# Performance work log

Hardware: AMD Instinct MI355X
Metric: run time of the kernel (lower is better)

Reference implementation:

```python
import jax, jax.numpy as jnp
import numpy as np

N_NODES = 50000
N_EDGES = 600000
H_DIM = 128
BN_EPS = 1e-5


def setup_inputs() -> dict:
    key = jax.random.key(0)
    k1, k2, k3, k4 = jax.random.split(key, 4)
    ent_emb = jax.random.normal(k1, (N_NODES, H_DIM), dtype=jnp.float32)
    # xavier_normal_ init for the 128x128 weight
    std = float(np.sqrt(2.0 / (H_DIM + H_DIM)))
    neigh_w = jax.random.normal(k2, (H_DIM, H_DIM), dtype=jnp.float32) * std
    gamma = jnp.ones((H_DIM,), dtype=jnp.float32)
    beta = jnp.zeros((H_DIM,), dtype=jnp.float32)
    src = jax.random.randint(k3, (N_EDGES,), 0, N_NODES, dtype=jnp.int32)
    dst = jax.random.randint(k4, (N_EDGES,), 0, N_NODES, dtype=jnp.int32)
    return {"ent_emb": ent_emb, "neigh_w": neigh_w, "gamma": gamma,
            "beta": beta, "src": src, "dst": dst}


def reference(ent_emb, neigh_w, gamma, beta, src, dst):
    # Edge dot-product scores: u_dot_v('emb','emb')  -> [E]
    e_src = ent_emb[src]                      # [E, H]
    e_dst = ent_emb[dst]                      # [E, H]
    scores = jnp.sum(e_src * e_dst, axis=-1)  # [E]

    # edge_softmax: softmax over incoming edges of each destination node
    seg_max = jax.ops.segment_max(scores, dst, num_segments=N_NODES)
    seg_max = jnp.where(jnp.isfinite(seg_max), seg_max, 0.0)  # nodes w/o edges
    e = jnp.exp(scores - seg_max[dst])                         # [E]
    seg_sum = jax.ops.segment_sum(e, dst, num_segments=N_NODES)
    norm = e / seg_sum[dst]                                    # [E]

    # update_all(u_mul_e, sum): weighted gather-sum aggregation
    msg = e_src * norm[:, None]                                # [E, H]
    neigh = jax.ops.segment_sum(msg, dst, num_segments=N_NODES)  # [N, H]

    # matmul + BatchNorm1d (training-mode batch stats) + tanh
    h = neigh @ neigh_w                                        # [N, H]
    mean = jnp.mean(h, axis=0)
    var = jnp.var(h, axis=0)  # biased, matches torch BN normalization
    h = (h - mean) * jax.lax.rsqrt(var + BN_EPS) * gamma + beta
    return jnp.tanh(h)
```

## Files before the change

### kernel.cpp

```cpp
#include <hip/hip_runtime.h>
#include <hip/hip_fp16.h>
#include <math.h>

#define N_NODES 50000
#define N_EDGES 600000
#define H 128
#define BN_EPS 1e-5f
#define MAXDEG 48

__global__ void k_scatter(const int* __restrict__ src, const int* __restrict__ dst,
                          int* __restrict__ cnt, int* __restrict__ slots) {
    int i = blockIdx.x * blockDim.x + threadIdx.x;
    if (i < N_EDGES) {
        int d = dst[i];
        int pos = atomicAdd(cnt + d, 1);
        if (pos < MAXDEG) slots[d * MAXDEG + pos] = src[i];
    }
}

#define F4SCALE(a, s) { (a).x *= (s); (a).y *= (s); (a).z *= (s); (a).w *= (s); }
#define F4FMA(a, e, v) { (a).x += (e)*(v).x; (a).y += (e)*(v).y; (a).z += (e)*(v).z; (a).w += (e)*(v).w; }
#define F4SHFLADD(a, msk) { (a).x += __shfl_xor((a).x, msk, 64); (a).y += __shfl_xor((a).y, msk, 64); \
                            (a).z += __shfl_xor((a).z, msk, 64); (a).w += __shfl_xor((a).w, msk, 64); }

__global__ __launch_bounds__(256) void k_fused(const float* __restrict__ emb,
                                               const int* __restrict__ cnt,
                                               const int* __restrict__ slots,
                                               float* __restrict__ neigh) {
    int wid = (blockIdx.x * blockDim.x + threadIdx.x) >> 6;
    int lane = threadIdx.x & 63;
    if (wid >= N_NODES) return;
    int g = lane >> 3;
    int l = lane & 7;

    int deg = min(cnt[wid], MAXDEG);
    int sid = slots[wid * MAXDEG + min(lane, MAXDEG - 1)];

    const float4* rd = (const float4*)(emb + (size_t)wid * H) + l * 4;
    float4 b0 = rd[0], b1 = rd[1], b2 = rd[2], b3 = rd[3];

    float m = -INFINITY, ssum = 0.0f;
    float4 acc0 = {0,0,0,0}, acc1 = {0,0,0,0}, acc2 = {0,0,0,0}, acc3 = {0,0,0,0};

    for (int cb = 0; cb < deg; cb += 8) {
        int e = cb + g;
        bool valid = e < deg;
        int s = __shfl(sid, valid ? e : 0, 64);
        const float4* rs = (const float4*)(emb + (size_t)s * H) + l * 4;
        float4 a0 = rs[0], a1 = rs[1], a2 = rs[2], a3 = rs[3];

        float v = a0.x*b0.x + a0.y*b0.y + a0.z*b0.z + a0.w*b0.w
                + a1.x*b1.x + a1.y*b1.y + a1.z*b1.z + a1.w*b1.w
                + a2.x*b2.x + a2.y*b2.y + a2.z*b2.z + a2.w*b2.w
                + a3.x*b3.x + a3.y*b3.y + a3.z*b3.z + a3.w*b3.w;
        v += __shfl_xor(v, 1, 64);
        v += __shfl_xor(v, 2, 64);
        v += __shfl_xor(v, 4, 64);
        if (!valid) v = -INFINITY;

        float cmax = v;
        cmax = fmaxf(cmax, __shfl_xor(cmax, 8, 64));
        cmax = fmaxf(cmax, __shfl_xor(cmax, 16, 64));
        cmax = fmaxf(cmax, __shfl_xor(cmax, 32, 64));
        float mnew = fmaxf(m, cmax);
        if (mnew > m) {
            float scale = __expf(m - mnew);
            ssum *= scale;
            F4SCALE(acc0, scale); F4SCALE(acc1, scale);
            F4SCALE(acc2, scale); F4SCALE(acc3, scale);
            m = mnew;
        }

        float ev = __expf(v - m);
        ssum += ev;
        F4FMA(acc0, ev, a0); F4FMA(acc1, ev, a1);
        F4FMA(acc2, ev, a2); F4FMA(acc3, ev, a3);
    }

    ssum += __shfl_xor(ssum, 8, 64);
    ssum += __shfl_xor(ssum, 16, 64);
    ssum += __shfl_xor(ssum, 32, 64);
    F4SHFLADD(acc0, 8);  F4SHFLADD(acc1, 8);  F4SHFLADD(acc2, 8);  F4SHFLADD(acc3, 8);
    F4SHFLADD(acc0, 16); F4SHFLADD(acc1, 16); F4SHFLADD(acc2, 16); F4SHFLADD(acc3, 16);
    F4SHFLADD(acc0, 32); F4SHFLADD(acc1, 32); F4SHFLADD(acc2, 32); F4SHFLADD(acc3, 32);

    float inv = (deg > 0) ? 1.0f / ssum : 0.0f;
    if (g == 0) {
        float4* po = (float4*)(neigh + (size_t)wid * H) + l * 4;
        F4SCALE(acc0, inv); F4SCALE(acc1, inv); F4SCALE(acc2, inv); F4SCALE(acc3, inv);
        po[0] = acc0; po[1] = acc1; po[2] = acc2; po[3] = acc3;
    }
}

#define MM_ROWS 128
#define MM_COLS 64
template <bool F16>
__global__ __launch_bounds__(256, 4) void k_matmul(const float* __restrict__ neigh,
                                                   const float* __restrict__ W,
                                                   float* __restrict__ hout32,
                                                   __half* __restrict__ hout16,
                                                   float* __restrict__ stats) {
    __shared__ float Wl[H * MM_COLS];
    __shared__ float Sl[16 * MM_COLS];
    __shared__ float Ql[16 * MM_COLS];
    int t = threadIdx.x;
    int bc = blockIdx.x & 1;
    int br = blockIdx.x >> 1;
    int c0 = bc * MM_COLS;
    int n0 = br * MM_ROWS;
    int cg = t & 15, rg = t >> 4;
    int j0 = cg * 4;
    int r0 = n0 + rg * 8;

    for (int idx = t; idx < H * 16; idx += 256) {
        int k = idx >> 4, c4 = idx & 15;
        *(float4*)&Wl[k * MM_COLS + c4 * 4] =
            *((const float4*)(W + (size_t)k * H + c0) + c4);
    }

    const float* pr[8];
    bool valid[8];
#pragma unroll
    for (int i = 0; i < 8; ++i) {
        int n = r0 + i;
        valid[i] = (n < N_NODES);
        pr[i] = neigh + (size_t)(valid[i] ? n : 0) * H;
    }

    __syncthreads();

    float acc[8][4] = {};
    for (int k0 = 0; k0 < H; k0 += 4) {
        float4 rv[8];
#pragma unroll
        for (int i = 0; i < 8; ++i) rv[i] = *(const float4*)(pr[i] + k0);
        float4 wv[4];
#pragma unroll
        for (int kk = 0; kk < 4; ++kk) wv[kk] = *(const float4*)&Wl[(k0 + kk) * MM_COLS + j0];
#pragma unroll
        for (int kk = 0; kk < 4; ++kk) {
#pragma unroll
            for (int i = 0; i < 8; ++i) {
                float rk = ((const float*)&rv[i])[kk];
                acc[i][0] += rk * wv[kk].x;
                acc[i][1] += rk * wv[kk].y;
                acc[i][2] += rk * wv[kk].z;
                acc[i][3] += rk * wv[kk].w;
            }
        }
    }

#pragma unroll
    for (int i = 0; i < 8; ++i) {
        if (valid[i]) {
            if (F16) {
                __half2 h01 = __floats2half2_rn(acc[i][0], acc[i][1]);
                __half2 h23 = __floats2half2_rn(acc[i][2], acc[i][3]);
                __half2* p = (__half2*)(hout16 + (size_t)(r0 + i) * H + c0 + j0);
                p[0] = h01; p[1] = h23;
            } else {
                float4 o = make_float4(acc[i][0], acc[i][1], acc[i][2], acc[i][3]);
                *(float4*)(hout32 + (size_t)(r0 + i) * H + c0 + j0) = o;
            }
        }
    }

#pragma unroll
    for (int c = 0; c < 4; ++c) {
        float s = 0.0f, q = 0.0f;
#pragma unroll
        for (int i = 0; i < 8; ++i) {
            if (valid[i]) { s += acc[i][c]; q += acc[i][c] * acc[i][c]; }
        }
        Sl[rg * MM_COLS + j0 + c] = s;
        Ql[rg * MM_COLS + j0 + c] = q;
    }
    __syncthreads();
    if (t < MM_COLS) {
        float s = 0.0f;
#pragma unroll
        for (int r = 0; r < 16; ++r) s += Sl[r * MM_COLS + t];
        atomicAdd(stats + c0 + t, s);
    } else if (t < 2 * MM_COLS) {
        int j = t - MM_COLS;
        float q = 0.0f;
#pragma unroll
        for (int r = 0; r < 16; ++r) q += Ql[r * MM_COLS + j];
        atomicAdd(stats + 128 + c0 + j, q);
    }
}

__device__ __forceinline__ float tanh_fast(float x) {
    float e = __expf(2.0f * x);
    return 1.0f - 2.0f / (e + 1.0f);
}

__global__ __launch_bounds__(256) void k_apply_f32(float* __restrict__ h,
                                                   const float* __restrict__ stats,
                                                   const float* __restrict__ gamma,
                                                   const float* __restrict__ beta) {
    __shared__ float sc[128], sh[128];
    int t = threadIdx.x;
    if (t < 128) {
        float mean = stats[t] * (1.0f / N_NODES);
        float var = stats[128 + t] * (1.0f / N_NODES) - mean * mean;
        var = fmaxf(var, 0.0f);
        float s = gamma[t] * rsqrtf(var + BN_EPS);
        sc[t] = s;
        sh[t] = beta[t] - mean * s;
    }
    __syncthreads();
    int i = blockIdx.x * 256 + t;
    if (i < N_NODES * H / 4) {
        float4 v = ((const float4*)h)[i];
        int jb = (i & 31) * 4;
        v.x = tanh_fast(v.x * sc[jb]     + sh[jb]);
        v.y = tanh_fast(v.y * sc[jb + 1] + sh[jb + 1]);
        v.z = tanh_fast(v.z * sc[jb + 2] + sh[jb + 2]);
        v.w = tanh_fast(v.w * sc[jb + 3] + sh[jb + 3]);
        ((float4*)h)[i] = v;
    }
}

__global__ __launch_bounds__(256) void k_apply_f16(const __half* __restrict__ h,
                                                   float* __restrict__ out,
                                                   const float* __restrict__ stats,
                                                   const float* __restrict__ gamma,
                                                   const float* __restrict__ beta) {
    __shared__ float sc[128], sh[128];
    int t = threadIdx.x;
    if (t < 128) {
        float mean = stats[t] * (1.0f / N_NODES);
        float var = stats[128 + t] * (1.0f / N_NODES) - mean * mean;
        var = fmaxf(var, 0.0f);
        float s = gamma[t] * rsqrtf(var + BN_EPS);
        sc[t] = s;
        sh[t] = beta[t] - mean * s;
    }
    __syncthreads();
    int i = blockIdx.x * 256 + t;
    if (i < N_NODES * H / 8) {
        union { uint4 u; __half2 h2[4]; } U;
        U.u = ((const uint4*)h)[i];
        int jb = (i & 15) * 8;
        float2 f0 = __half22float2(U.h2[0]);
        float2 f1 = __half22float2(U.h2[1]);
        float2 f2 = __half22float2(U.h2[2]);
        float2 f3 = __half22float2(U.h2[3]);
        float4 o0, o1;
        o0.x = tanh_fast(f0.x * sc[jb]     + sh[jb]);
        o0.y = tanh_fast(f0.y * sc[jb + 1] + sh[jb + 1]);
        o0.z = tanh_fast(f1.x * sc[jb + 2] + sh[jb + 2]);
        o0.w = tanh_fast(f1.y * sc[jb + 3] + sh[jb + 3]);
        o1.x = tanh_fast(f2.x * sc[jb + 4] + sh[jb + 4]);
        o1.y = tanh_fast(f2.y * sc[jb + 5] + sh[jb + 5]);
        o1.z = tanh_fast(f3.x * sc[jb + 6] + sh[jb + 6]);
        o1.w = tanh_fast(f3.y * sc[jb + 7] + sh[jb + 7]);
        ((float4*)out)[2 * i]     = o0;
        ((float4*)out)[2 * i + 1] = o1;
    }
}

extern "C" void kernel_launch(void* const* d_in, const int* in_sizes, int n_in,
                              void* d_out, int out_size, void* d_ws, size_t ws_size,
                              hipStream_t stream) {
    const float* emb   = (const float*)d_in[0];
    const float* W     = (const float*)d_in[1];
    const float* gamma = (const float*)d_in[2];
    const float* beta  = (const float*)d_in[3];
    const int*   src   = (const int*)d_in[4];
    const int*   dst   = (const int*)d_in[5];
    float* out = (float*)d_out;

    int*    cnt   = (int*)d_ws;
    float*  stats = (float*)(cnt + N_NODES);
    int*    slots = (int*)(stats + 256) + 4;
    float*  neigh = (float*)(slots + (size_t)N_NODES * MAXDEG);
    __half* hbuf  = (__half*)(neigh + (size_t)N_NODES * H);

    size_t need_f16 = (size_t)(N_NODES + 260) * 4
                    + (size_t)N_NODES * MAXDEG * 4
                    + (size_t)N_NODES * H * 4
                    + (size_t)N_NODES * H * 2;
    bool use_f16 = ws_size >= need_f16;

    hipMemsetAsync(cnt, 0, (N_NODES + 260) * sizeof(int), stream);
    k_scatter<<<(N_EDGES + 255) / 256, 256, 0, stream>>>(src, dst, cnt, slots);
    k_fused<<<(N_NODES * 64 + 255) / 256, 256, 0, stream>>>(emb, cnt, slots, neigh);

    int nblk_mm = ((N_NODES + MM_ROWS - 1) / MM_ROWS) * 2;
    if (use_f16) {
        k_matmul<true><<<nblk_mm, 256, 0, stream>>>(neigh, W, nullptr, hbuf, stats);
        k_apply_f16<<<(N_NODES * H / 8 + 255) / 256, 256, 0, stream>>>(hbuf, out, stats, gamma, beta);
    } else {
        k_matmul<false><<<nblk_mm, 256, 0, stream>>>(neigh, W, out, nullptr, stats);
        k_apply_f32<<<(N_NODES * H / 4 + 255) / 256, 256, 0, stream>>>(out, stats, gamma, beta);
    }
}
```

Measured before the change: 217.5 us.

## Compute all 128 output columns per matmul block to halve neigh reads

```diff
diff --git a/kernel.cpp b/kernel.cpp
--- a/kernel.cpp
+++ b/kernel.cpp
@@ -93,30 +93,21 @@
 }
 
 #define MM_ROWS 128
-#define MM_COLS 64
 template <bool F16>
-__global__ __launch_bounds__(256, 4) void k_matmul(const float* __restrict__ neigh,
+__global__ __launch_bounds__(256, 2) void k_matmul(const float* __restrict__ neigh,
                                                    const float* __restrict__ W,
                                                    float* __restrict__ hout32,
                                                    __half* __restrict__ hout16,
                                                    float* __restrict__ stats) {
-    __shared__ float Wl[H * MM_COLS];
-    __shared__ float Sl[16 * MM_COLS];
-    __shared__ float Ql[16 * MM_COLS];
+    __shared__ float Wl[H * H];
     int t = threadIdx.x;
-    int bc = blockIdx.x & 1;
-    int br = blockIdx.x >> 1;
-    int c0 = bc * MM_COLS;
-    int n0 = br * MM_ROWS;
+    int n0 = blockIdx.x * MM_ROWS;
     int cg = t & 15, rg = t >> 4;
-    int j0 = cg * 4;
+    int j0 = cg * 8;
     int r0 = n0 + rg * 8;
 
-    for (int idx = t; idx < H * 16; idx += 256) {
-        int k = idx >> 4, c4 = idx & 15;
-        *(float4*)&Wl[k * MM_COLS + c4 * 4] =
-            *((const float4*)(W + (size_t)k * H + c0) + c4);
-    }
+    for (int idx = t; idx < H * H / 4; idx += 256)
+        ((float4*)Wl)[idx] = ((const float4*)W)[idx];
 
     const float* pr[8];
     bool valid[8];
@@ -129,23 +120,30 @@
 
     __syncthreads();
 
-    float acc[8][4] = {};
+    float acc[8][8] = {};
     for (int k0 = 0; k0 < H; k0 += 4) {
         float4 rv[8];
 #pragma unroll
         for (int i = 0; i < 8; ++i) rv[i] = *(const float4*)(pr[i] + k0);
-        float4 wv[4];
-#pragma unroll
-        for (int kk = 0; kk < 4; ++kk) wv[kk] = *(const float4*)&Wl[(k0 + kk) * MM_COLS + j0];
+        float4 wa[4], wb[4];
+#pragma unroll
+        for (int kk = 0; kk < 4; ++kk) {
+            wa[kk] = *(const float4*)&Wl[(k0 + kk) * H + j0];
+            wb[kk] = *(const float4*)&Wl[(k0 + kk) * H + j0 + 4];
+        }
 #pragma unroll
         for (int kk = 0; kk < 4; ++kk) {
 #pragma unroll
             for (int i = 0; i < 8; ++i) {
                 float rk = ((const float*)&rv[i])[kk];
-                acc[i][0] += rk * wv[kk].x;
-                acc[i][1] += rk * wv[kk].y;
-                acc[i][2] += rk * wv[kk].z;
-                acc[i][3] += rk * wv[kk].w;
+                acc[i][0] += rk * wa[kk].x;
+                acc[i][1] += rk * wa[kk].y;
+                acc[i][2] += rk * wa[kk].z;
+                acc[i][3] += rk * wa[kk].w;
+                acc[i][4] += rk * wb[kk].x;
+                acc[i][5] += rk * wb[kk].y;
+                acc[i][6] += rk * wb[kk].z;
+                acc[i][7] += rk * wb[kk].w;
             }
         }
     }
@@ -154,39 +152,46 @@
     for (int i = 0; i < 8; ++i) {
         if (valid[i]) {
             if (F16) {
-                __half2 h01 = __floats2half2_rn(acc[i][0], acc[i][1]);
-                __half2 h23 = __floats2half2_rn(acc[i][2], acc[i][3]);
-                __half2* p = (__half2*)(hout16 + (size_t)(r0 + i) * H + c0 + j0);
-                p[0] = h01; p[1] = h23;
+                union { uint4 u; __half2 h2[4]; } U;
+                U.h2[0] = __floats2half2_rn(acc[i][0], acc[i][1]);
+                U.h2[1] = __floats2half2_rn(acc[i][2], acc[i][3]);
+                U.h2[2] = __floats2half2_rn(acc[i][4], acc[i][5]);
+                U.h2[3] = __floats2half2_rn(acc[i][6], acc[i][7]);
+                *(uint4*)(hout16 + (size_t)(r0 + i) * H + j0) = U.u;
             } else {
-                float4 o = make_float4(acc[i][0], acc[i][1], acc[i][2], acc[i][3]);
-                *(float4*)(hout32 + (size_t)(r0 + i) * H + c0 + j0) = o;
+                *(float4*)(hout32 + (size_t)(r0 + i) * H + j0) =
+                    make_float4(acc[i][0], acc[i][1], acc[i][2], acc[i][3]);
+                *(float4*)(hout32 + (size_t)(r0 + i) * H + j0 + 4) =
+                    make_float4(acc[i][4], acc[i][5], acc[i][6], acc[i][7]);
             }
         }
     }
 
-#pragma unroll
-    for (int c = 0; c < 4; ++c) {
+    __syncthreads();
+    float* Sl = Wl;
+    float* Ql = Wl + 16 * H;
+#pragma unroll
+    for (int c = 0; c < 8; ++c) {
         float s = 0.0f, q = 0.0f;
 #pragma unroll
         for (int i = 0; i < 8; ++i) {
             if (valid[i]) { s += acc[i][c]; q += acc[i][c] * acc[i][c]; }
         }
-        Sl[rg * MM_COLS + j0 + c] = s;
-        Ql[rg * MM_COLS + j0 + c] = q;
-    }
-    __syncthreads();
-    if (t < MM_COLS) {
+        Sl[rg * H + j0 + c] = s;
+        Ql[rg * H + j0 + c] = q;
+    }
+    __syncthreads();
+    if (t < H) {
         float s = 0.0f;
 #pragma unroll
-        for (int r = 0; r < 16; ++r) s += Sl[r * MM_COLS + t];
-        atomicAdd(stats + c0 + t, s);
-    } else if (t < 2 * MM_COLS) {
-        int j = t - MM_COLS;
+        for (int r = 0; r < 16; ++r) s += Sl[r * H + t];
+        atomicAdd(stats + t, s);
+    } else {
+        int j = t - H;
         float q = 0.0f;
 #pragma unroll
-        for (int r = 0; r < 16; ++r) q += Ql[r * MM_COLS + j];
-        atomicAdd(stats + 128 + c0 + j, q);
+        for (int r = 0; r < 16; ++r) q += Ql[r * H + j];
+        atomicAdd(stats + 128 + j, q);
     }
 }
 
@@ -288,7 +293,7 @@
     k_scatter<<<(N_EDGES + 255) / 256, 256, 0, stream>>>(src, dst, cnt, slots);
     k_fused<<<(N_NODES * 64 + 255) / 256, 256, 0, stream>>>(emb, cnt, slots, neigh);
 
-    int nblk_mm = ((N_NODES + MM_ROWS - 1) / MM_ROWS) * 2;
+    int nblk_mm = (N_NODES + MM_ROWS - 1) / MM_ROWS;
     if (use_f16) {
         k_matmul<true><<<nblk_mm, 256, 0, stream>>>(neigh, W, nullptr, hbuf, stats);
         k_apply_f16<<<(N_NODES * H / 8 + 255) / 256, 256, 0, stream>>>(hbuf, out, stats, gamma, beta);
```

After: 207.4 us. 1.05x faster.
